# Optimization experiments

Hardware: AMD Instinct MI355X
Metric: run time of the kernel (lower is better)

Reference implementation:

```python
import jax, jax.numpy as jnp
import numpy as np

N = 256                     # num_nodes
P = N * (N - 1) // 2        # undirected pairs (32640)
B = 32                      # batch size
H = 64                      # hidden_dim

# edge ordering matches the torch loops: for i<j append [i,j] then [j,i]
_iu = np.triu_indices(N, 1)
SRC_P = jnp.asarray(_iu[0])                                   # (P,) pair src i
DST_P = jnp.asarray(_iu[1])                                   # (P,) pair dst j
SRC_D = jnp.asarray(np.stack([_iu[0], _iu[1]], 1).ravel())    # (2P,) directed src, interleaved
DST_D = jnp.asarray(np.stack([_iu[1], _iu[0]], 1).ravel())    # (2P,) directed dst
# GCNConv adds self-loops internally
SRC_F = jnp.concatenate([SRC_D, jnp.arange(N)])               # (2P+N,)
DST_F = jnp.concatenate([DST_D, jnp.arange(N)])


def _glorot(key, fan_in, fan_out):
    s = (2.0 / (fan_in + fan_out)) ** 0.5
    return jax.random.normal(key, (fan_in, fan_out), dtype=jnp.float32) * s


def setup_inputs() -> dict:
    key = jax.random.key(0)
    ks = jax.random.split(key, 8)
    # edge decisions in {0, 0.5, 1}; one-hot current-edge indicator
    dec = jax.random.choice(ks[0], jnp.array([0.0, 0.5, 1.0], dtype=jnp.float32), (B, P))
    cur = jax.random.randint(ks[1], (B,), 0, P)
    ind = jax.nn.one_hot(cur, P, dtype=jnp.float32)
    x = jnp.concatenate([dec, ind], axis=1)                   # (B, 2P)
    return {
        "x": x,
        "W1": _glorot(ks[2], 3, H), "b1": jnp.zeros((H,), jnp.float32),
        "W2": _glorot(ks[3], H, H), "b2": jnp.zeros((H,), jnp.float32),
        "W3": _glorot(ks[4], H, H), "b3": jnp.zeros((H,), jnp.float32),
        "We1": _glorot(ks[5], 2 * H + 3, H), "be1": jnp.zeros((H,), jnp.float32),
        "We2": _glorot(ks[6], H, 1), "be2": jnp.zeros((1,), jnp.float32),
    }


def _gcn_conv(h, W, b, norm):
    # h: (B, N, Fin) -> (B, N, Fout); symmetric-normalized gather-scatter over
    # the complete graph + self loops (all GCN degrees equal N here).
    hw = h @ W                                                # (B, N, Fout)
    msg = hw[:, SRC_F, :] * norm[None, :, None]               # (B, 2P+N, Fout)
    agg = jnp.zeros_like(hw).at[:, DST_F, :].add(msg)         # scatter-add
    return agg + b


def reference(x, W1, b1, W2, b2, W3, b3, We1, be1, We2, be2):
    dec = x[:, :P]                                            # (B, P) edge decisions
    ind = x[:, P:]                                            # (B, P) current-edge indicator

    # per-pair edge features, duplicated for both directed copies (interleaved)
    ef = jnp.stack([(dec == 1.0).astype(x.dtype),
                    (dec != 0.5).astype(x.dtype),
                    ind], axis=-1)                            # (B, P, 3)
    ea = jnp.repeat(ef, 2, axis=1)                            # (B, 2P, 3)

    # node degrees under the decided adjacency (decision == 1 pairs)
    a_rep = jnp.repeat((dec == 1.0).astype(x.dtype), 2, axis=1)   # (B, 2P)
    deg = jnp.zeros((x.shape[0], N), x.dtype).at[:, DST_D].add(a_rep)

    cur = jnp.argmax(ind, axis=1)                             # (B,)
    i_node = SRC_P[cur]
    j_node = DST_P[cur]
    bidx = jnp.arange(x.shape[0])
    attached = (jnp.zeros((x.shape[0], N), x.dtype)
                .at[bidx, i_node].set(1.0)
                .at[bidx, j_node].set(1.0))

    node_feat = jnp.stack([deg / (N - 1),
                           (deg == 0.0).astype(x.dtype),
                           attached], axis=-1)                # (B, N, 3)

    # GCN normalization on complete graph + self loops: every degree == N
    deg_gcn = jnp.zeros((N,), x.dtype).at[DST_F].add(1.0)
    norm = jax.lax.rsqrt(deg_gcn[SRC_F] * deg_gcn[DST_F])     # (2P+N,), all 1/N

    h = jax.nn.relu(_gcn_conv(node_feat, W1, b1, norm))
    h = jax.nn.relu(_gcn_conv(h, W2, b2, norm))
    h = jax.nn.relu(_gcn_conv(h, W3, b3, norm))               # (B, N, H)

    # edge head: gather endpoints + edge attrs -> MLP
    rep = jnp.concatenate([h[:, SRC_D, :], h[:, DST_D, :], ea], axis=-1)  # (B, 2P, 2H+3)
    hm = jax.nn.relu(rep @ We1 + be1)
    logits = (hm @ We2 + be2)[..., 0]                         # (B, 2P)

    # select the two directed copies of the current edge (fixed-shape mask)
    sel = jnp.stack([2 * cur, 2 * cur + 1], axis=1)           # (B, 2)
    return jax.nn.sigmoid(jnp.take_along_axis(logits, sel, axis=1))
```

## Files before the change

### kernel.cpp

```cpp
#include <hip/hip_runtime.h>
#include <math.h>

#define NN 256
#define PP 32640
#define HH 64
#define BB 32
#define SPLIT 32
#define NF4 (PP / 4)
#define F4_PER (NF4 / SPLIT)


__global__ __launch_bounds__(256) void gnn_scan(
    const float* __restrict__ x,
    unsigned int* __restrict__ ws_mask,
    int* __restrict__ ws_cnt,
    int* __restrict__ ws_cur)
{
    const int blk   = blockIdx.x;
    const int b     = blk >> 5;
    const int chunk = blk & (SPLIT - 1);
    const int tid   = threadIdx.x;
    const int lane  = tid & 63;
    const int w     = tid >> 6;

    __shared__ unsigned char touched[NN];
    __shared__ int wcnt[4];
    touched[tid] = 0;
    __syncthreads();

    const float*  decp = x + (size_t)b * (2 * PP);
    const float4* dec4 = (const float4*)decp;
    const float4* ind4 = (const float4*)(decp + PP);

    int cnt = 0;
    if (tid < F4_PER) {
        const int q  = chunk * F4_PER + tid;
        float4 d  = dec4[q];
        float4 iv = ind4[q];
        const int p0 = q * 4;

        int i = (int)((511.0f - sqrtf(261121.0f - 8.0f * (float)p0)) * 0.5f);
        while (i * (511 - i) / 2 > p0) --i;
        while ((i + 1) * (510 - i) / 2 <= p0) ++i;
        int rowStart = i * (511 - i) / 2;

        float dv[4]  = {d.x, d.y, d.z, d.w};
        float ivv[4] = {iv.x, iv.y, iv.z, iv.w};
        #pragma unroll
        for (int u = 0; u < 4; ++u) {
            const int p = p0 + u;
            while (p - rowStart >= 255 - i) { ++i; rowStart = i * (511 - i) / 2; }
            if (ivv[u] > 0.5f) ws_cur[b] = p;
            if (dv[u] == 1.0f) {
                const int j = i + 1 + (p - rowStart);
                touched[i] = 1;
                touched[j] = 1;
                ++cnt;
            }
        }
    }
    __syncthreads();

    const bool bit = touched[tid] != 0;
    unsigned long long m = __ballot(bit);
    if (lane == 0) {
        ws_mask[blk * 8 + w * 2 + 0] = (unsigned int)m;
        ws_mask[blk * 8 + w * 2 + 1] = (unsigned int)(m >> 32);
    }
    #pragma unroll
    for (int off = 32; off > 0; off >>= 1) cnt += __shfl_down(cnt, off);
    if (lane == 0) wcnt[w] = cnt;
    __syncthreads();
    if (tid == 0) ws_cnt[blk] = wcnt[0] + wcnt[1] + wcnt[2] + wcnt[3];
}

__global__ __launch_bounds__(256) void gnn_epilogue(
    const float* __restrict__ x,
    const float* __restrict__ W1, const float* __restrict__ b1,
    const float* __restrict__ W2, const float* __restrict__ b2,
    const float* __restrict__ W3, const float* __restrict__ b3,
    const float* __restrict__ We1, const float* __restrict__ be1,
    const float* __restrict__ We2, const float* __restrict__ be2,
    const unsigned int* __restrict__ ws_mask,
    const int* __restrict__ ws_cnt,
    const int* __restrict__ ws_cur,
    float* __restrict__ out)
{
    const int b    = blockIdx.x;
    const int tid  = threadIdx.x;
    const int lane = tid & 63;
    const int w    = tid >> 6;

    __shared__ float gS[HH];
    __shared__ float p[4][HH];
    __shared__ unsigned int mw[SPLIT * 8];
    __shared__ int s_pop, s_cnt;

    if (tid == 0) s_pop = 0;
    mw[tid] = ws_mask[b * (SPLIT * 8) + tid];
    const int cv   = (tid < SPLIT) ? ws_cnt[b * SPLIT + tid] : 0;
    const int cur  = ws_cur[b];
    const float dcur = x[(size_t)b * (2 * PP) + cur];
    __syncthreads();

    if (tid < 8) {
        unsigned int o = 0;
        #pragma unroll
        for (int c = 0; c < SPLIT; ++c) o |= mw[c * 8 + tid];
        atomicAdd(&s_pop, __popc(o));
    }
    if (w == 0) {
        int s = cv;
        #pragma unroll
        for (int off = 32; off > 0; off >>= 1) s += __shfl_down(s, off);
        if (lane == 0) s_cnt = s;
    }
    __syncthreads();

    const float f0 = (float)(2 * s_cnt) * (1.0f / 255.0f);
    const float f1 = (float)(NN - s_pop);

    if (tid < HH) {
        float s = f0 * W1[tid] + f1 * W1[HH + tid] + 2.0f * W1[2 * HH + tid];
        gS[tid] = fmaxf(s * (1.0f / 256.0f) + b1[tid], 0.0f);
    }
    __syncthreads();

    {
        float s = 0.0f;
        const float* Wp = W2 + (w * 16) * HH + lane;
        #pragma unroll
        for (int kk = 0; kk < 16; ++kk) s += gS[w * 16 + kk] * Wp[kk * HH];
        p[w][lane] = s;
    }
    __syncthreads();
    if (tid < HH)
        gS[tid] = fmaxf(p[0][tid] + p[1][tid] + p[2][tid] + p[3][tid] + b2[tid], 0.0f);
    __syncthreads();

    {
        float s = 0.0f;
        const float* Wp = W3 + (w * 16) * HH + lane;
        #pragma unroll
        for (int kk = 0; kk < 16; ++kk) s += gS[w * 16 + kk] * Wp[kk * HH];
        p[w][lane] = s;
    }
    __syncthreads();
    if (tid < HH)
        gS[tid] = fmaxf(p[0][tid] + p[1][tid] + p[2][tid] + p[3][tid] + b3[tid], 0.0f);
    __syncthreads();

    {
        float s = 0.0f;
        const float* Wa = We1 + (w * 16) * HH + lane;
        const float* Wb = We1 + (64 + w * 16) * HH + lane;
        #pragma unroll
        for (int kk = 0; kk < 16; ++kk)
            s += gS[w * 16 + kk] * (Wa[kk * HH] + Wb[kk * HH]);
        p[w][lane] = s;
    }
    __syncthreads();
    if (tid < HH) {
        const float e0 = (dcur == 1.0f) ? 1.0f : 0.0f;
        const float e1 = (dcur != 0.5f) ? 1.0f : 0.0f;
        float v = p[0][tid] + p[1][tid] + p[2][tid] + p[3][tid] + be1[tid]
                + e0 * We1[128 * HH + tid] + e1 * We1[129 * HH + tid]
                + We1[130 * HH + tid];
        v = fmaxf(v, 0.0f);

        float contrib = v * We2[tid];
        #pragma unroll
        for (int off = 32; off > 0; off >>= 1)
            contrib += __shfl_down(contrib, off);

        if (tid == 0) {
            const float sig = 1.0f / (1.0f + expf(-(contrib + be2[0])));
            out[b * 2 + 0] = sig;
            out[b * 2 + 1] = sig;
        }
    }
}

extern "C" void kernel_launch(void* const* d_in, const int* in_sizes, int n_in,
                              void* d_out, int out_size, void* d_ws, size_t ws_size,
                              hipStream_t stream) {
    const float* x   = (const float*)d_in[0];
    const float* W1  = (const float*)d_in[1];
    const float* b1  = (const float*)d_in[2];
    const float* W2  = (const float*)d_in[3];
    const float* b2  = (const float*)d_in[4];
    const float* W3  = (const float*)d_in[5];
    const float* b3  = (const float*)d_in[6];
    const float* We1 = (const float*)d_in[7];
    const float* be1 = (const float*)d_in[8];
    const float* We2 = (const float*)d_in[9];
    const float* be2 = (const float*)d_in[10];
    float* out = (float*)d_out;

    unsigned int* ws_mask = (unsigned int*)d_ws;
    int* ws_cnt = (int*)(ws_mask + (size_t)BB * SPLIT * 8);
    int* ws_cur = ws_cnt + (size_t)BB * SPLIT;

    gnn_scan<<<BB * SPLIT, 256, 0, stream>>>(x, ws_mask, ws_cnt, ws_cur);
    gnn_epilogue<<<BB, 256, 0, stream>>>(x, W1, b1, W2, b2, W3, b3,
                                         We1, be1, We2, be2,
                                         ws_mask, ws_cnt, ws_cur, out);
}
```

Before: 13.82 us.

## Fuse scan and epilogue into one kernel with one block per batch

Merges the split scan kernel and the epilogue kernel into a single launch with one 1024-thread block per batch element. Per-chunk partial masks, counts and current-edge index now stay in shared memory, removing the workspace round trip and the second launch. In exchange, the scan of each batch row uses only one block per row (32 blocks total), reducing memory-level parallelism across the GPU.

```diff
diff --git a/kernel.cpp b/kernel.cpp
--- a/kernel.cpp
+++ b/kernel.cpp
@@ -5,27 +5,29 @@
 #define PP 32640
 #define HH 64
 #define BB 32
-#define SPLIT 32
 #define NF4 (PP / 4)
-#define F4_PER (NF4 / SPLIT)
 
-
-__global__ __launch_bounds__(256) void gnn_scan(
+__global__ __launch_bounds__(1024) void gnn_fused(
     const float* __restrict__ x,
-    unsigned int* __restrict__ ws_mask,
-    int* __restrict__ ws_cnt,
-    int* __restrict__ ws_cur)
+    const float* __restrict__ W1, const float* __restrict__ b1,
+    const float* __restrict__ W2, const float* __restrict__ b2,
+    const float* __restrict__ W3, const float* __restrict__ b3,
+    const float* __restrict__ We1, const float* __restrict__ be1,
+    const float* __restrict__ We2, const float* __restrict__ be2,
+    float* __restrict__ out)
 {
-    const int blk   = blockIdx.x;
-    const int b     = blk >> 5;
-    const int chunk = blk & (SPLIT - 1);
-    const int tid   = threadIdx.x;
-    const int lane  = tid & 63;
-    const int w     = tid >> 6;
+    const int b    = blockIdx.x;
+    const int tid  = threadIdx.x;
+    const int lane = tid & 63;
+    const int w    = tid >> 6;
 
     __shared__ unsigned char touched[NN];
-    __shared__ int wcnt[4];
-    touched[tid] = 0;
+    __shared__ float gS[HH];
+    __shared__ float pr[4][HH];
+    __shared__ int   s_cur, s_cnt, s_pop;
+
+    if (tid < NN) touched[tid] = 0;
+    if (tid == 0) { s_cur = 0; s_cnt = 0; s_pop = 0; }
     __syncthreads();
 
     const float*  decp = x + (size_t)b * (2 * PP);
@@ -33,8 +35,7 @@
     const float4* ind4 = (const float4*)(decp + PP);
 
     int cnt = 0;
-    if (tid < F4_PER) {
-        const int q  = chunk * F4_PER + tid;
+    for (int q = tid; q < NF4; q += 1024) {
         float4 d  = dec4[q];
         float4 iv = ind4[q];
         const int p0 = q * 4;
@@ -50,7 +51,7 @@
         for (int u = 0; u < 4; ++u) {
             const int p = p0 + u;
             while (p - rowStart >= 255 - i) { ++i; rowStart = i * (511 - i) / 2; }
-            if (ivv[u] > 0.5f) ws_cur[b] = p;
+            if (ivv[u] > 0.5f) s_cur = p;
             if (dv[u] == 1.0f) {
                 const int j = i + 1 + (p - rowStart);
                 touched[i] = 1;
@@ -59,61 +60,15 @@
             }
         }
     }
+
+    #pragma unroll
+    for (int off = 32; off > 0; off >>= 1) cnt += __shfl_down(cnt, off);
+    if (lane == 0) atomicAdd(&s_cnt, cnt);
     __syncthreads();
 
-    const bool bit = touched[tid] != 0;
-    unsigned long long m = __ballot(bit);
-    if (lane == 0) {
-        ws_mask[blk * 8 + w * 2 + 0] = (unsigned int)m;
-        ws_mask[blk * 8 + w * 2 + 1] = (unsigned int)(m >> 32);
-    }
-    #pragma unroll
-    for (int off = 32; off > 0; off >>= 1) cnt += __shfl_down(cnt, off);
-    if (lane == 0) wcnt[w] = cnt;
-    __syncthreads();
-    if (tid == 0) ws_cnt[blk] = wcnt[0] + wcnt[1] + wcnt[2] + wcnt[3];
-}
-
-__global__ __launch_bounds__(256) void gnn_epilogue(
-    const float* __restrict__ x,
-    const float* __restrict__ W1, const float* __restrict__ b1,
-    const float* __restrict__ W2, const float* __restrict__ b2,
-    const float* __restrict__ W3, const float* __restrict__ b3,
-    const float* __restrict__ We1, const float* __restrict__ be1,
-    const float* __restrict__ We2, const float* __restrict__ be2,
-    const unsigned int* __restrict__ ws_mask,
-    const int* __restrict__ ws_cnt,
-    const int* __restrict__ ws_cur,
-    float* __restrict__ out)
-{
-    const int b    = blockIdx.x;
-    const int tid  = threadIdx.x;
-    const int lane = tid & 63;
-    const int w    = tid >> 6;
-
-    __shared__ float gS[HH];
-    __shared__ float p[4][HH];
-    __shared__ unsigned int mw[SPLIT * 8];
-    __shared__ int s_pop, s_cnt;
-
-    if (tid == 0) s_pop = 0;
-    mw[tid] = ws_mask[b * (SPLIT * 8) + tid];
-    const int cv   = (tid < SPLIT) ? ws_cnt[b * SPLIT + tid] : 0;
-    const int cur  = ws_cur[b];
-    const float dcur = x[(size_t)b * (2 * PP) + cur];
-    __syncthreads();
-
-    if (tid < 8) {
-        unsigned int o = 0;
-        #pragma unroll
-        for (int c = 0; c < SPLIT; ++c) o |= mw[c * 8 + tid];
-        atomicAdd(&s_pop, __popc(o));
-    }
-    if (w == 0) {
-        int s = cv;
-        #pragma unroll
-        for (int off = 32; off > 0; off >>= 1) s += __shfl_down(s, off);
-        if (lane == 0) s_cnt = s;
+    if (tid < NN) {
+        unsigned long long m = __ballot(touched[tid] != 0);
+        if (lane == 0) atomicAdd(&s_pop, __popcll(m));
     }
     __syncthreads();
 
@@ -126,44 +81,45 @@
     }
     __syncthreads();
 
-    {
+    if (tid < 256) {
         float s = 0.0f;
         const float* Wp = W2 + (w * 16) * HH + lane;
         #pragma unroll
         for (int kk = 0; kk < 16; ++kk) s += gS[w * 16 + kk] * Wp[kk * HH];
-        p[w][lane] = s;
+        pr[w][lane] = s;
     }
     __syncthreads();
     if (tid < HH)
-        gS[tid] = fmaxf(p[0][tid] + p[1][tid] + p[2][tid] + p[3][tid] + b2[tid], 0.0f);
+        gS[tid] = fmaxf(pr[0][tid] + pr[1][tid] + pr[2][tid] + pr[3][tid] + b2[tid], 0.0f);
     __syncthreads();
 
-    {
+    if (tid < 256) {
         float s = 0.0f;
         const float* Wp = W3 + (w * 16) * HH + lane;
         #pragma unroll
         for (int kk = 0; kk < 16; ++kk) s += gS[w * 16 + kk] * Wp[kk * HH];
-        p[w][lane] = s;
+        pr[w][lane] = s;
     }
     __syncthreads();
     if (tid < HH)
-        gS[tid] = fmaxf(p[0][tid] + p[1][tid] + p[2][tid] + p[3][tid] + b3[tid], 0.0f);
+        gS[tid] = fmaxf(pr[0][tid] + pr[1][tid] + pr[2][tid] + pr[3][tid] + b3[tid], 0.0f);
     __syncthreads();
 
-    {
+    if (tid < 256) {
         float s = 0.0f;
         const float* Wa = We1 + (w * 16) * HH + lane;
         const float* Wb = We1 + (64 + w * 16) * HH + lane;
         #pragma unroll
         for (int kk = 0; kk < 16; ++kk)
             s += gS[w * 16 + kk] * (Wa[kk * HH] + Wb[kk * HH]);
-        p[w][lane] = s;
+        pr[w][lane] = s;
     }
     __syncthreads();
     if (tid < HH) {
+        const float dcur = decp[s_cur];
         const float e0 = (dcur == 1.0f) ? 1.0f : 0.0f;
         const float e1 = (dcur != 0.5f) ? 1.0f : 0.0f;
-        float v = p[0][tid] + p[1][tid] + p[2][tid] + p[3][tid] + be1[tid]
+        float v = pr[0][tid] + pr[1][tid] + pr[2][tid] + pr[3][tid] + be1[tid]
                 + e0 * We1[128 * HH + tid] + e1 * We1[129 * HH + tid]
                 + We1[130 * HH + tid];
         v = fmaxf(v, 0.0f);
@@ -197,12 +153,6 @@
     const float* be2 = (const float*)d_in[10];
     float* out = (float*)d_out;
 
-    unsigned int* ws_mask = (unsigned int*)d_ws;
-    int* ws_cnt = (int*)(ws_mask + (size_t)BB * SPLIT * 8);
-    int* ws_cur = ws_cnt + (size_t)BB * SPLIT;
-
-    gnn_scan<<<BB * SPLIT, 256, 0, stream>>>(x, ws_mask, ws_cnt, ws_cur);
-    gnn_epilogue<<<BB, 256, 0, stream>>>(x, W1, b1, W2, b2, W3, b3,
-                                         We1, be1, We2, be2,
-                                         ws_mask, ws_cnt, ws_cur, out);
+    gnn_fused<<<BB, 1024, 0, stream>>>(x, W1, b1, W2, b2, W3, b3,
+                                       We1, be1, We2, be2, out);
 }
```

New measurement: 15.24 us. 10.3% more time.

## Shrink epilogue to one wavefront with shuffle-based reductions and matvecs

Applied to the files above, without the earlier changes.

The epilogue kernel now runs one 64-thread wavefront per batch, replacing shared-memory staging and block barriers with cross-lane shuffles for the mask OR, popcount, count reduction and the three 64x64 matvecs. The scan kernel now encodes the current edge's decision flags directly, so the epilogue no longer needs a dependent load from x. In exchange, each thread runs 64-step serial dot products instead of 16-step partial sums across four waves, which lengthens the per-thread dependency chain.

```diff
diff --git a/kernel.cpp b/kernel.cpp
--- a/kernel.cpp
+++ b/kernel.cpp
@@ -14,7 +14,7 @@
     const float* __restrict__ x,
     unsigned int* __restrict__ ws_mask,
     int* __restrict__ ws_cnt,
-    int* __restrict__ ws_cur)
+    unsigned int* __restrict__ ws_e01)
 {
     const int blk   = blockIdx.x;
     const int b     = blk >> 5;
@@ -50,7 +50,9 @@
         for (int u = 0; u < 4; ++u) {
             const int p = p0 + u;
             while (p - rowStart >= 255 - i) { ++i; rowStart = i * (511 - i) / 2; }
-            if (ivv[u] > 0.5f) ws_cur[b] = p;
+            if (ivv[u] > 0.5f) {
+                ws_e01[b] = (dv[u] == 1.0f ? 1u : 0u) | (dv[u] != 0.5f ? 2u : 0u);
+            }
             if (dv[u] == 1.0f) {
                 const int j = i + 1 + (p - rowStart);
                 touched[i] = 1;
@@ -61,8 +63,7 @@
     }
     __syncthreads();
 
-    const bool bit = touched[tid] != 0;
-    unsigned long long m = __ballot(bit);
+    unsigned long long m = __ballot(touched[tid] != 0);
     if (lane == 0) {
         ws_mask[blk * 8 + w * 2 + 0] = (unsigned int)m;
         ws_mask[blk * 8 + w * 2 + 1] = (unsigned int)(m >> 32);
@@ -74,8 +75,7 @@
     if (tid == 0) ws_cnt[blk] = wcnt[0] + wcnt[1] + wcnt[2] + wcnt[3];
 }
 
-__global__ __launch_bounds__(256) void gnn_epilogue(
-    const float* __restrict__ x,
+__global__ __launch_bounds__(64) void gnn_epilogue(
     const float* __restrict__ W1, const float* __restrict__ b1,
     const float* __restrict__ W2, const float* __restrict__ b2,
     const float* __restrict__ W3, const float* __restrict__ b3,
@@ -83,101 +83,65 @@
     const float* __restrict__ We2, const float* __restrict__ be2,
     const unsigned int* __restrict__ ws_mask,
     const int* __restrict__ ws_cnt,
-    const int* __restrict__ ws_cur,
+    const unsigned int* __restrict__ ws_e01,
     float* __restrict__ out)
 {
-    const int b    = blockIdx.x;
-    const int tid  = threadIdx.x;
-    const int lane = tid & 63;
-    const int w    = tid >> 6;
+    const int b = blockIdx.x;
+    const int o = threadIdx.x;
 
-    __shared__ float gS[HH];
-    __shared__ float p[4][HH];
-    __shared__ unsigned int mw[SPLIT * 8];
-    __shared__ int s_pop, s_cnt;
+    const uint4* mp = (const uint4*)(ws_mask + (size_t)b * (SPLIT * 8));
+    uint4 m = mp[o];
+    #pragma unroll
+    for (int off = 2; off < 64; off <<= 1) {
+        m.x |= __shfl_xor(m.x, off);
+        m.y |= __shfl_xor(m.y, off);
+        m.z |= __shfl_xor(m.z, off);
+        m.w |= __shfl_xor(m.w, off);
+    }
+    int p = __popc(m.x) + __popc(m.y) + __popc(m.z) + __popc(m.w);
+    p += __shfl_xor(p, 1);
+    const int pop = __shfl(p, 0);
 
-    if (tid == 0) s_pop = 0;
-    mw[tid] = ws_mask[b * (SPLIT * 8) + tid];
-    const int cv   = (tid < SPLIT) ? ws_cnt[b * SPLIT + tid] : 0;
-    const int cur  = ws_cur[b];
-    const float dcur = x[(size_t)b * (2 * PP) + cur];
-    __syncthreads();
+    int c = (o < SPLIT) ? ws_cnt[b * SPLIT + o] : 0;
+    #pragma unroll
+    for (int off = 1; off < 32; off <<= 1) c += __shfl_xor(c, off);
+    const int scnt = __shfl(c, 0);
 
-    if (tid < 8) {
-        unsigned int o = 0;
-        #pragma unroll
-        for (int c = 0; c < SPLIT; ++c) o |= mw[c * 8 + tid];
-        atomicAdd(&s_pop, __popc(o));
-    }
-    if (w == 0) {
-        int s = cv;
-        #pragma unroll
-        for (int off = 32; off > 0; off >>= 1) s += __shfl_down(s, off);
-        if (lane == 0) s_cnt = s;
-    }
-    __syncthreads();
+    const unsigned int se = ws_e01[b];
+    const float e0 = (float)(se & 1u);
+    const float e1 = (float)((se >> 1) & 1u);
 
-    const float f0 = (float)(2 * s_cnt) * (1.0f / 255.0f);
-    const float f1 = (float)(NN - s_pop);
+    const float f0 = (float)(2 * scnt) * (1.0f / 255.0f);
+    const float f1 = (float)(NN - pop);
 
-    if (tid < HH) {
-        float s = f0 * W1[tid] + f1 * W1[HH + tid] + 2.0f * W1[2 * HH + tid];
-        gS[tid] = fmaxf(s * (1.0f / 256.0f) + b1[tid], 0.0f);
-    }
-    __syncthreads();
+    float g = fmaxf((f0 * W1[o] + f1 * W1[HH + o] + 2.0f * W1[2 * HH + o])
+                    * (1.0f / 256.0f) + b1[o], 0.0f);
 
-    {
-        float s = 0.0f;
-        const float* Wp = W2 + (w * 16) * HH + lane;
-        #pragma unroll
-        for (int kk = 0; kk < 16; ++kk) s += gS[w * 16 + kk] * Wp[kk * HH];
-        p[w][lane] = s;
-    }
-    __syncthreads();
-    if (tid < HH)
-        gS[tid] = fmaxf(p[0][tid] + p[1][tid] + p[2][tid] + p[3][tid] + b2[tid], 0.0f);
-    __syncthreads();
+    float acc = b2[o];
+    #pragma unroll
+    for (int k = 0; k < HH; ++k) acc += __shfl(g, k) * W2[k * HH + o];
+    g = fmaxf(acc, 0.0f);
 
-    {
-        float s = 0.0f;
-        const float* Wp = W3 + (w * 16) * HH + lane;
-        #pragma unroll
-        for (int kk = 0; kk < 16; ++kk) s += gS[w * 16 + kk] * Wp[kk * HH];
-        p[w][lane] = s;
-    }
-    __syncthreads();
-    if (tid < HH)
-        gS[tid] = fmaxf(p[0][tid] + p[1][tid] + p[2][tid] + p[3][tid] + b3[tid], 0.0f);
-    __syncthreads();
+    acc = b3[o];
+    #pragma unroll
+    for (int k = 0; k < HH; ++k) acc += __shfl(g, k) * W3[k * HH + o];
+    g = fmaxf(acc, 0.0f);
 
-    {
-        float s = 0.0f;
-        const float* Wa = We1 + (w * 16) * HH + lane;
-        const float* Wb = We1 + (64 + w * 16) * HH + lane;
-        #pragma unroll
-        for (int kk = 0; kk < 16; ++kk)
-            s += gS[w * 16 + kk] * (Wa[kk * HH] + Wb[kk * HH]);
-        p[w][lane] = s;
-    }
-    __syncthreads();
-    if (tid < HH) {
-        const float e0 = (dcur == 1.0f) ? 1.0f : 0.0f;
-        const float e1 = (dcur != 0.5f) ? 1.0f : 0.0f;
-        float v = p[0][tid] + p[1][tid] + p[2][tid] + p[3][tid] + be1[tid]
-                + e0 * We1[128 * HH + tid] + e1 * We1[129 * HH + tid]
-                + We1[130 * HH + tid];
-        v = fmaxf(v, 0.0f);
+    acc = be1[o] + e0 * We1[128 * HH + o] + e1 * We1[129 * HH + o] + We1[130 * HH + o];
+    #pragma unroll
+    for (int k = 0; k < HH; ++k)
+        acc += __shfl(g, k) * (We1[k * HH + o] + We1[(HH + k) * HH + o]);
+    const float hm = fmaxf(acc, 0.0f);
 
-        float contrib = v * We2[tid];
-        #pragma unroll
-        for (int off = 32; off > 0; off >>= 1)
-            contrib += __shfl_down(contrib, off);
+    float contrib = hm * We2[o];
+    #pragma unroll
+    for (int off = 32; off > 0; off >>= 1)
+        contrib += __shfl_down(contrib, off);
 
-        if (tid == 0) {
-            const float sig = 1.0f / (1.0f + expf(-(contrib + be2[0])));
-            out[b * 2 + 0] = sig;
-            out[b * 2 + 1] = sig;
-        }
+    if (o == 0) {
+        const float sig = 1.0f / (1.0f + expf(-(contrib + be2[0])));
+        out[b * 2 + 0] = sig;
+        out[b * 2 + 1] = sig;
     }
 }
 
@@ -199,10 +163,10 @@
 
     unsigned int* ws_mask = (unsigned int*)d_ws;
     int* ws_cnt = (int*)(ws_mask + (size_t)BB * SPLIT * 8);
-    int* ws_cur = ws_cnt + (size_t)BB * SPLIT;
+    unsigned int* ws_e01 = (unsigned int*)(ws_cnt + BB * SPLIT);
 
-    gnn_scan<<<BB * SPLIT, 256, 0, stream>>>(x, ws_mask, ws_cnt, ws_cur);
-    gnn_epilogue<<<BB, 256, 0, stream>>>(x, W1, b1, W2, b2, W3, b3,
-                                         We1, be1, We2, be2,
-                                         ws_mask, ws_cnt, ws_cur, out);
+    gnn_scan<<<BB * SPLIT, 256, 0, stream>>>(x, ws_mask, ws_cnt, ws_e01);
+    gnn_epilogue<<<BB, 64, 0, stream>>>(W1, b1, W2, b2, W3, b3,
+                                        We1, be1, We2, be2,
+                                        ws_mask, ws_cnt, ws_e01, out);
 }
```

Measured after the change: 15.56 us. +12.5%, slower.
